# Optimization experiments

Measured on AMD Instinct MI355X. Metric: run time of the kernel, lower is better.

The kernel has to match this reference:

```python
import jax, jax.numpy as jnp
import numpy as np

N, E, DIM, H, EDIM = 50000, 800000, 128, 4, 16
C = DIM // H  # per-head channels = 32

def _ln(x, g, b, eps=1e-5):
    mu = jnp.mean(x, -1, keepdims=True)
    var = jnp.mean((x - mu) ** 2, -1, keepdims=True)
    return (x - mu) * jax.lax.rsqrt(var + eps) * g + b

def setup_inputs() -> dict:
    key = jax.random.key(0)
    ks = jax.random.split(key, 16)
    s = lambda d: 1.0 / np.sqrt(d)
    inp = {
        'x': jax.random.normal(ks[0], (N, DIM), jnp.float32),
        'edge_index_s': jax.random.randint(ks[1], (2, E), 0, N, jnp.int64),
        'edge_attr_s': jax.random.normal(ks[2], (E, EDIM), jnp.float32),
        'Wq': jax.random.normal(ks[3], (DIM, DIM), jnp.float32) * s(DIM),
        'bq': jnp.zeros((DIM,), jnp.float32),
        'Wk': jax.random.normal(ks[4], (DIM, DIM), jnp.float32) * s(DIM),
        'bk': jnp.zeros((DIM,), jnp.float32),
        'Wv': jax.random.normal(ks[5], (DIM, DIM), jnp.float32) * s(DIM),
        'bv': jnp.zeros((DIM,), jnp.float32),
        'We': jax.random.normal(ks[6], (EDIM, DIM), jnp.float32) * s(EDIM),
        'be': jnp.zeros((DIM,), jnp.float32),
        'Ws': jax.random.normal(ks[7], (DIM, DIM), jnp.float32) * s(DIM),
        'bs': jnp.zeros((DIM,), jnp.float32),
        'Wbeta': jax.random.normal(ks[8], (3 * DIM, 1), jnp.float32) * s(3 * DIM),
        'g1': jnp.ones((DIM,), jnp.float32),
        'b1': jnp.zeros((DIM,), jnp.float32),
        'Wf1': jax.random.normal(ks[9], (DIM, 4 * DIM), jnp.float32) * s(DIM),
        'bf1': jnp.zeros((4 * DIM,), jnp.float32),
        'Wf2': jax.random.normal(ks[10], (4 * DIM, DIM), jnp.float32) * s(4 * DIM),
        'bf2': jnp.zeros((DIM,), jnp.float32),
        'g2': jnp.ones((DIM,), jnp.float32),
        'b2': jnp.zeros((DIM,), jnp.float32),
    }
    return inp

def reference(x, edge_index_s, edge_attr_s, Wq, bq, Wk, bk, Wv, bv, We, be,
              Ws, bs, Wbeta, g1, b1, Wf1, bf1, Wf2, bf2, g2, b2):
    src, dst = edge_index_s[0], edge_index_s[1]
    # project + reshape to [N, H, C]
    q = (x @ Wq + bq).reshape(N, H, C)
    k = (x @ Wk + bk).reshape(N, H, C)
    v = (x @ Wv + bv).reshape(N, H, C)
    e = (edge_attr_s @ We + be).reshape(E, H, C)
    # gather along edges (irregular access)
    kj = k[src] + e  # [E, H, C]
    vj = v[src] + e
    alpha = jnp.einsum('ehc,ehc->eh', q[dst], kj) / jnp.sqrt(jnp.float32(C))
    # segment softmax over incoming edges of each dst node
    m = jax.ops.segment_max(alpha, dst, num_segments=N)  # [N, H]
    a = jnp.exp(alpha - m[dst])
    denom = jax.ops.segment_sum(a, dst, num_segments=N)
    a = a / (denom[dst] + 1e-16)
    out = jax.ops.segment_sum(a[:, :, None] * vj, dst, num_segments=N)  # [N, H, C]
    out = out.reshape(N, DIM)
    # beta-gated skip (TransformerConv beta=True)
    xr = x @ Ws + bs
    beta = jax.nn.sigmoid(jnp.concatenate([out, xr, out - xr], -1) @ Wbeta)  # [N, 1]
    xs = beta * xr + (1.0 - beta) * out
    # residual + LN + FFN + LN
    h = _ln(x + xs, g1, b1)
    ff = jax.nn.relu(h @ Wf1 + bf1) @ Wf2 + bf2
    return _ln(h + ff, g2, b2)
```

## Files before the change

### kernel.cpp

```cpp
#include <hip/hip_runtime.h>
#include <hip/hip_bf16.h>

#define NN 50000
#define EE 800000
#define DIMM 128

typedef __attribute__((ext_vector_type(8))) short bf16x8;
typedef __attribute__((ext_vector_type(8))) unsigned short us8;
typedef __attribute__((ext_vector_type(4))) float f32x4;

static __device__ __forceinline__ unsigned short f2bf(float f) {
    unsigned int u = __float_as_uint(f);
    unsigned int r = (u + 0x7fffu + ((u >> 16) & 1u)) >> 16;
    return (unsigned short)r;
}
static __device__ __forceinline__ float bf2f(unsigned short s) {
    return __uint_as_float(((unsigned int)s) << 16);
}

#define RED16(v) do { int _t; \
    _t = __builtin_amdgcn_update_dpp(0, __float_as_int(v), 0x128, 0xF, 0xF, true); v += __int_as_float(_t); \
    _t = __builtin_amdgcn_update_dpp(0, __float_as_int(v), 0x124, 0xF, 0xF, true); v += __int_as_float(_t); \
    _t = __builtin_amdgcn_update_dpp(0, __float_as_int(v), 0x122, 0xF, 0xF, true); v += __int_as_float(_t); \
    _t = __builtin_amdgcn_update_dpp(0, __float_as_int(v), 0x121, 0xF, 0xF, true); v += __int_as_float(_t); \
} while (0)

__global__ __launch_bounds__(256) void pack_w(
    const float* __restrict__ Wq, const float* __restrict__ Wk,
    const float* __restrict__ Wv, const float* __restrict__ Ws,
    const float* __restrict__ bq, const float* __restrict__ bk,
    const float* __restrict__ bv, const float* __restrict__ bs,
    const float* __restrict__ Wf1, const float* __restrict__ Wf2,
    unsigned short* __restrict__ wqkvsT, unsigned short* __restrict__ wf1T,
    unsigned short* __restrict__ wf2T, float* __restrict__ biasq)
{
    int i = blockIdx.x * 256 + threadIdx.x;
    if (i < 65536) {
        int n = i >> 7, k = i & 127;
        int sel = n >> 7, col = n & 127;
        const float* W = sel == 0 ? Wq : sel == 1 ? Wk : sel == 2 ? Wv : Ws;
        wqkvsT[i] = f2bf(W[k * 128 + col]);
    } else if (i < 131072) {
        int j = i - 65536; int n = j >> 7, k = j & 127;
        wf1T[j] = f2bf(Wf1[k * 512 + n]);
    } else if (i < 196608) {
        int j = i - 131072; int n = j >> 9, k = j & 511;
        wf2T[j] = f2bf(Wf2[k * 128 + n]);
    } else if (i < 197120) {
        int j = i - 196608; int sel = j >> 7;
        const float* bp = sel == 0 ? bq : sel == 1 ? bk : sel == 2 ? bv : bs;
        biasq[j] = bp[j & 127];
    }
}

template<bool A_BF16, int EPI>
__global__ __launch_bounds__(256) void gemm_k(
    const void* __restrict__ Ap, const unsigned short* __restrict__ Bt,
    const float* __restrict__ bias, void* __restrict__ Cp,
    float* __restrict__ qb, unsigned short* __restrict__ kvb, float* __restrict__ xrb,
    int M, int Nn, int K)
{
    __shared__ unsigned short As[128][72];
    __shared__ unsigned short Bs[128][72];
    int tid = threadIdx.x;
    int nb = Nn >> 7;
    int bm = blockIdx.x / nb, bn = blockIdx.x % nb;
    int w = tid >> 6, lane = tid & 63;
    int wm = w >> 1, wn = w & 1;
    int lr = lane & 15, quad = lane >> 4;

    f32x4 acc[4][4];
    #pragma unroll
    for (int i = 0; i < 4; i++)
        #pragma unroll
        for (int j = 0; j < 4; j++) { f32x4 z = {0.f, 0.f, 0.f, 0.f}; acc[i][j] = z; }

    for (int kc = 0; kc < K; kc += 64) {
        #pragma unroll
        for (int it = 0; it < 4; ++it) {
            int row = it * 32 + (tid >> 3);
            int k8 = (tid & 7) * 8;
            int rg = bm * 128 + row;
            us8 st = {0, 0, 0, 0, 0, 0, 0, 0};
            if (rg < M) {
                if constexpr (A_BF16) {
                    st = *(const us8*)((const unsigned short*)Ap + (size_t)rg * K + kc + k8);
                } else {
                    const float* src = (const float*)Ap + (size_t)rg * K + kc + k8;
                    float4 f0 = *(const float4*)src;
                    float4 f1 = *(const float4*)(src + 4);
                    st[0] = f2bf(f0.x); st[1] = f2bf(f0.y); st[2] = f2bf(f0.z); st[3] = f2bf(f0.w);
                    st[4] = f2bf(f1.x); st[5] = f2bf(f1.y); st[6] = f2bf(f1.z); st[7] = f2bf(f1.w);
                }
            }
            *(us8*)&As[row][k8] = st;
            *(us8*)&Bs[row][k8] = *(const us8*)(Bt + (size_t)(bn * 128 + row) * K + kc + k8);
        }
        __syncthreads();
        #pragma unroll
        for (int kk = 0; kk < 2; ++kk) {
            bf16x8 af[4], bfr[4];
            #pragma unroll
            for (int mi = 0; mi < 4; mi++)
                af[mi] = *(const bf16x8*)&As[wm * 64 + mi * 16 + lr][kk * 32 + quad * 8];
            #pragma unroll
            for (int ni = 0; ni < 4; ni++)
                bfr[ni] = *(const bf16x8*)&Bs[wn * 64 + ni * 16 + lr][kk * 32 + quad * 8];
            #pragma unroll
            for (int mi = 0; mi < 4; mi++)
                #pragma unroll
                for (int ni = 0; ni < 4; ni++)
                    acc[mi][ni] = __builtin_amdgcn_mfma_f32_16x16x32_bf16(af[mi], bfr[ni], acc[mi][ni], 0, 0, 0);
        }
        __syncthreads();
    }
    #pragma unroll
    for (int mi = 0; mi < 4; mi++) {
        #pragma unroll
        for (int ni = 0; ni < 4; ni++) {
            int cg = bn * 128 + wn * 64 + ni * 16 + lr;
            float bv = bias[cg];
            #pragma unroll
            for (int r = 0; r < 4; r++) {
                int rg = bm * 128 + wm * 64 + mi * 16 + quad * 4 + r;
                if (rg < M) {
                    float val = acc[mi][ni][r] + bv;
                    if constexpr (EPI == 0) {
                        ((float*)Cp)[(size_t)rg * Nn + cg] = val;
                    } else if constexpr (EPI == 1) {
                        val = fmaxf(val, 0.f);
                        ((unsigned short*)Cp)[(size_t)rg * Nn + cg] = f2bf(val);
                    } else {
                        int sel = cg >> 7, c = cg & 127;
                        if (sel == 0)      qb[(size_t)rg * 128 + c] = val;
                        else if (sel == 1) kvb[(size_t)rg * 256 + 2 * c] = f2bf(val);
                        else if (sel == 2) kvb[(size_t)rg * 256 + 2 * c + 1] = f2bf(val);
                        else               xrb[(size_t)rg * 128 + c] = val;
                    }
                }
            }
        }
    }
}

__global__ __launch_bounds__(256) void qwe_k(
    const float* __restrict__ q, const float* __restrict__ We,
    float* __restrict__ qweb)
{
    int wave = threadIdx.x >> 6, lane = threadIdx.x & 63;
    int n = blockIdx.x * 4 + wave;
    if (n >= NN) return;
    int head = lane >> 4, j = lane & 15;
    const float* qp = q + (size_t)n * 128 + head * 32;
    const float* wp = We + j * 128 + head * 32;
    float acc = 0.f;
    #pragma unroll
    for (int c = 0; c < 32; c += 4) {
        float4 qv = *(const float4*)(qp + c);
        float4 wv = *(const float4*)(wp + c);
        acc += qv.x * wv.x + qv.y * wv.y + qv.z * wv.z + qv.w * wv.w;
    }
    qweb[(size_t)n * 64 + lane] = acc * 0.17677669529663687f;
}

__global__ __launch_bounds__(256) void hist_k(const int* __restrict__ dst, int* __restrict__ deg) {
    int e = blockIdx.x * 256 + threadIdx.x;
    if (e < EE) atomicAdd(&deg[dst[e]], 1);
}

__global__ __launch_bounds__(256) void scan_phaseA(const int* __restrict__ deg, int* __restrict__ rs,
                                                   int* __restrict__ bsum) {
    __shared__ int sm[256];
    int tid = threadIdx.x;
    int i = blockIdx.x * 256 + tid;
    int v = (i < NN) ? deg[i] : 0;
    sm[tid] = v;
    __syncthreads();
    #pragma unroll
    for (int off = 1; off < 256; off <<= 1) {
        int t = 0;
        if (tid >= off) t = sm[tid - off];
        __syncthreads();
        if (tid >= off) sm[tid] += t;
        __syncthreads();
    }
    if (i < NN) rs[i] = sm[tid] - v;
    if (tid == 255) bsum[blockIdx.x] = sm[255];
}

__global__ __launch_bounds__(256) void scan_phaseB(int* __restrict__ bsum, int nb) {
    __shared__ int sm[256];
    int tid = threadIdx.x;
    int v = (tid < nb) ? bsum[tid] : 0;
    sm[tid] = v;
    __syncthreads();
    #pragma unroll
    for (int off = 1; off < 256; off <<= 1) {
        int t = 0;
        if (tid >= off) t = sm[tid - off];
        __syncthreads();
        if (tid >= off) sm[tid] += t;
        __syncthreads();
    }
    if (tid < nb) bsum[tid] = sm[tid] - v;
}

__global__ __launch_bounds__(256) void scan_phaseC(int* __restrict__ rs, const int* __restrict__ bsum) {
    int i = blockIdx.x * 256 + threadIdx.x;
    if (i < NN) rs[i] += bsum[blockIdx.x];
    if (i == 0) rs[NN] = EE;
}

__global__ __launch_bounds__(256) void scatter_k(
    const int* __restrict__ src, const int* __restrict__ dst,
    const float* __restrict__ eattr, const int* __restrict__ rs,
    int* __restrict__ cur, int* __restrict__ srcs_sorted,
    unsigned short* __restrict__ eas)
{
    int e = blockIdx.x * 256 + threadIdx.x;
    if (e < EE) {
        int d = dst[e];
        int p = atomicAdd(&cur[d], 1);
        int pos = rs[d] + p;
        srcs_sorted[pos] = src[e];
        const float* ap = eattr + (size_t)e * 16;
        float4 a0 = *(const float4*)ap;
        float4 a1 = *(const float4*)(ap + 4);
        float4 a2 = *(const float4*)(ap + 8);
        float4 a3 = *(const float4*)(ap + 12);
        us8 lo, hi;
        lo[0] = f2bf(a0.x); lo[1] = f2bf(a0.y); lo[2] = f2bf(a0.z); lo[3] = f2bf(a0.w);
        lo[4] = f2bf(a1.x); lo[5] = f2bf(a1.y); lo[6] = f2bf(a1.z); lo[7] = f2bf(a1.w);
        hi[0] = f2bf(a2.x); hi[1] = f2bf(a2.y); hi[2] = f2bf(a2.z); hi[3] = f2bf(a2.w);
        hi[4] = f2bf(a3.x); hi[5] = f2bf(a3.y); hi[6] = f2bf(a3.z); hi[7] = f2bf(a3.w);
        *(us8*)(eas + (size_t)pos * 16)     = lo;
        *(us8*)(eas + (size_t)pos * 16 + 8) = hi;
    }
}

__global__ __launch_bounds__(256, 4) void attn_kernel(
    const float* __restrict__ q, const unsigned int* __restrict__ kvb,
    const float* __restrict__ xr, const float* __restrict__ x,
    const unsigned short* __restrict__ eas, const int* __restrict__ srcs,
    const int* __restrict__ rs, const float* __restrict__ qweb,
    const float* __restrict__ We, const float* __restrict__ be,
    const float* __restrict__ Wbeta,
    const float* __restrict__ gamma1, const float* __restrict__ beta1,
    float* __restrict__ hout, unsigned int* __restrict__ hbf)
{
    int wave = threadIdx.x >> 6;
    int lane = threadIdx.x & 63;
    int n = blockIdx.x * 4 + wave;
    if (n >= NN) return;
    int c0 = lane * 2, c1 = c0 + 1;
    int jlane = lane & 15;
    int hbase = lane & 48;

    float be0 = be[c0], be1 = be[c1];

    float2 q2 = *(const float2*)(q + (size_t)n * 128 + c0);
    q2.x *= 0.17677669529663687f;
    q2.y *= 0.17677669529663687f;

    float qbe = q2.x * be0 + q2.y * be1;
    RED16(qbe);
    float qwe = qweb[(size_t)n * 64 + lane];

    float l = 0.f, a0 = 0.f, a1 = 0.f, s = 0.f;
    int beg = rs[n], end = rs[n + 1];

    int sr0[8], sr1[8];
    unsigned short ea0[8], ea1[8];
    uint2 kv0[8], kv1[8];

#define LOADMETA(g, SR, EA) { \
    _Pragma("unroll") \
    for (int j = 0; j < 8; j++) { \
        int idx = min((g) + j, EE - 1); \
        SR[j] = srcs[idx]; \
        EA[j] = eas[(size_t)idx * 16 + jlane]; \
    } }
#define GATHER(SR, KV) { \
    _Pragma("unroll") \
    for (int j = 0; j < 8; j++) \
        KV[j] = *(const uint2*)(kvb + (size_t)SR[j] * 128 + (lane << 1)); }
#define COMPUTE(g, EA, KV) { \
    int cnt = end - (g); \
    _Pragma("unroll") \
    for (int j = 0; j < 8; j++) { \
        if (j < cnt) { \
            float ea = bf2f(EA[j]); \
            unsigned int kx = KV[j].x, ky = KV[j].y; \
            float k0 = __uint_as_float(kx << 16); \
            float v0 = __uint_as_float(kx & 0xffff0000u); \
            float k1 = __uint_as_float(ky << 16); \
            float v1 = __uint_as_float(ky & 0xffff0000u); \
            float part = fmaf(q2.x, k0, fmaf(q2.y, k1, qwe * ea)); \
            RED16(part); \
            float wgt = __expf(part + qbe); \
            l += wgt; \
            a0 = fmaf(wgt, v0, a0); \
            a1 = fmaf(wgt, v1, a1); \
            s = fmaf(wgt, ea, s); \
        } } }

    if (beg < end) {
        LOADMETA(beg, sr0, ea0)
        GATHER(sr0, kv0)
        for (int g = beg; ; g += 16) {
            bool m1 = (g + 8 < end);
            if (m1) { LOADMETA(g + 8, sr1, ea1) GATHER(sr1, kv1) }
            COMPUTE(g, ea0, kv0)
            if (!m1) break;
            bool m2 = (g + 16 < end);
            if (m2) { LOADMETA(g + 16, sr0, ea0) GATHER(sr0, kv0) }
            COMPUTE(g + 8, ea1, kv1)
            if (!m2) break;
        }
    }
#undef LOADMETA
#undef GATHER
#undef COMPUTE

    float eo0 = l * be0, eo1 = l * be1;
    #pragma unroll
    for (int j = 0; j < 16; j++) {
        float sj = __shfl(s, hbase + j);
        eo0 = fmaf(sj, We[j * 128 + c0], eo0);
        eo1 = fmaf(sj, We[j * 128 + c1], eo1);
    }
    a0 += eo0; a1 += eo1;

    float inv = l > 0.f ? 1.f / l : 0.f;
    float o0 = a0 * inv, o1 = a1 * inv;

    float wbo0 = Wbeta[c0],        wbo1 = Wbeta[c1];
    float wbx0 = Wbeta[128 + c0],  wbx1 = Wbeta[128 + c1];
    float wbd0 = Wbeta[256 + c0],  wbd1 = Wbeta[256 + c1];
    float2 xr2 = *(const float2*)(xr + (size_t)n * 128 + c0);
    float bl = o0 * wbo0 + o1 * wbo1 + xr2.x * wbx0 + xr2.y * wbx1
             + (o0 - xr2.x) * wbd0 + (o1 - xr2.y) * wbd1;
    #pragma unroll
    for (int off = 1; off < 64; off <<= 1) bl += __shfl_xor(bl, off);
    float beta = 1.f / (1.f + __expf(-bl));
    float xs0 = beta * xr2.x + (1.f - beta) * o0;
    float xs1 = beta * xr2.y + (1.f - beta) * o1;

    float2 xv = *(const float2*)(x + (size_t)n * 128 + c0);
    float t0 = xv.x + xs0, t1 = xv.y + xs1;
    float sm = t0 + t1;
    #pragma unroll
    for (int off = 1; off < 64; off <<= 1) sm += __shfl_xor(sm, off);
    float mu = sm * (1.f / 128.f);
    float d0 = t0 - mu, d1 = t1 - mu;
    float vv = d0 * d0 + d1 * d1;
    #pragma unroll
    for (int off = 1; off < 64; off <<= 1) vv += __shfl_xor(vv, off);
    float is = rsqrtf(vv * (1.f / 128.f) + 1e-5f);
    float h0 = d0 * is * gamma1[c0] + beta1[c0];
    float h1 = d1 * is * gamma1[c1] + beta1[c1];
    *(float2*)(hout + (size_t)n * 128 + c0) = make_float2(h0, h1);
    hbf[(size_t)n * 64 + lane] = (unsigned int)f2bf(h0) | ((unsigned int)f2bf(h1) << 16);
}

__global__ __launch_bounds__(256) void ln2_k(
    const float* __restrict__ h, const float* __restrict__ ff2,
    const float* __restrict__ gamma2, const float* __restrict__ beta2,
    float* __restrict__ out)
{
    int wave = threadIdx.x >> 6;
    int lane = threadIdx.x & 63;
    int n = blockIdx.x * 4 + wave;
    if (n >= NN) return;
    int c0 = lane * 2;
    float2 hv = *(const float2*)(h + (size_t)n * 128 + c0);
    float2 fv = *(const float2*)(ff2 + (size_t)n * 128 + c0);
    float t0 = hv.x + fv.x, t1 = hv.y + fv.y;
    float sm = t0 + t1;
    #pragma unroll
    for (int off = 1; off < 64; off <<= 1) sm += __shfl_xor(sm, off);
    float mu = sm * (1.f / 128.f);
    float d0 = t0 - mu, d1 = t1 - mu;
    float vv = d0 * d0 + d1 * d1;
    #pragma unroll
    for (int off = 1; off < 64; off <<= 1) vv += __shfl_xor(vv, off);
    float is = rsqrtf(vv * (1.f / 128.f) + 1e-5f);
    float o0 = d0 * is * gamma2[c0] + beta2[c0];
    float o1 = d1 * is * gamma2[c0 + 1] + beta2[c0 + 1];
    *(float2*)(out + (size_t)n * 128 + c0) = make_float2(o0, o1);
}

extern "C" void kernel_launch(void* const* d_in, const int* in_sizes, int n_in,
                              void* d_out, int out_size, void* d_ws, size_t ws_size,
                              hipStream_t stream) {
    const float* x      = (const float*)d_in[0];
    const int*   eindex = (const int*)d_in[1];
    const float* eattr  = (const float*)d_in[2];
    const float* Wq = (const float*)d_in[3];  const float* bq = (const float*)d_in[4];
    const float* Wk = (const float*)d_in[5];  const float* bk = (const float*)d_in[6];
    const float* Wv = (const float*)d_in[7];  const float* bv = (const float*)d_in[8];
    const float* We = (const float*)d_in[9];  const float* be = (const float*)d_in[10];
    const float* Ws = (const float*)d_in[11]; const float* bs = (const float*)d_in[12];
    const float* Wbeta = (const float*)d_in[13];
    const float* g1 = (const float*)d_in[14]; const float* b1 = (const float*)d_in[15];
    const float* Wf1 = (const float*)d_in[16]; const float* bf1 = (const float*)d_in[17];
    const float* Wf2 = (const float*)d_in[18]; const float* bf2 = (const float*)d_in[19];
    const float* g2 = (const float*)d_in[20]; const float* b2 = (const float*)d_in[21];

    char* ws = (char*)d_ws;
    size_t off = 0;
    #define ALLOC(ptr, type, bytes) type* ptr = (type*)(ws + off); off = (off + (size_t)(bytes) + 255) & ~(size_t)255;
    ALLOC(wqkvsT, unsigned short, 512 * 128 * 2)
    ALLOC(wf1T,   unsigned short, 512 * 128 * 2)
    ALLOC(wf2T,   unsigned short, 128 * 512 * 2)
    ALLOC(biasq,  float,          512 * 4)
    ALLOC(qb,     float,          (size_t)NN * 128 * 4)
    ALLOC(kvb,    unsigned short, (size_t)NN * 256 * 2)
    ALLOC(xrb,    float,          (size_t)NN * 128 * 4)
    ALLOC(h,      float,          (size_t)NN * 128 * 4)
    ALLOC(hbf,    unsigned int,   (size_t)NN * 128 * 2)
    ALLOC(qweb,   float,          (size_t)NN * 64 * 4)
    ALLOC(deg,    int,            2 * NN * 4)
    ALLOC(row_start, int,         (NN + 1) * 4)
    ALLOC(bsum,   int,            1024)
    ALLOC(srcs_sorted, int,       (size_t)EE * 4)
    ALLOC(eas,    unsigned short, (size_t)EE * 16 * 2)
    #undef ALLOC
    int* cursor = deg + NN;
    unsigned short* ff1 = (unsigned short*)qb;
    float* ff2 = xrb;

    hipMemsetAsync(deg, 0, (size_t)2 * NN * 4, stream);

    pack_w<<<770, 256, 0, stream>>>(Wq, Wk, Wv, Ws, bq, bk, bv, bs, Wf1, Wf2,
                                    wqkvsT, wf1T, wf2T, biasq);

    gemm_k<false, 2><<<391 * 4, 256, 0, stream>>>(x, wqkvsT, biasq, nullptr,
                                                  qb, kvb, xrb, NN, 512, 128);

    qwe_k<<<12500, 256, 0, stream>>>(qb, We, qweb);

    hist_k<<<3125, 256, 0, stream>>>(eindex + EE, deg);
    scan_phaseA<<<196, 256, 0, stream>>>(deg, row_start, bsum);
    scan_phaseB<<<1, 256, 0, stream>>>(bsum, 196);
    scan_phaseC<<<196, 256, 0, stream>>>(row_start, bsum);
    scatter_k<<<3125, 256, 0, stream>>>(eindex, eindex + EE, eattr, row_start,
                                        cursor, srcs_sorted, eas);

    attn_kernel<<<12500, 256, 0, stream>>>(qb, (const unsigned int*)kvb, xrb, x,
                                           eas, srcs_sorted, row_start, qweb,
                                           We, be, Wbeta, g1, b1, h, hbf);

    gemm_k<true, 1><<<391 * 4, 256, 0, stream>>>(hbf, wf1T, bf1, ff1,
                                                 nullptr, nullptr, nullptr, NN, 512, 128);
    gemm_k<true, 0><<<391 * 1, 256, 0, stream>>>(ff1, wf2T, bf2, ff2,
                                                 nullptr, nullptr, nullptr, NN, 128, 512);

    ln2_k<<<12500, 256, 0, stream>>>(h, ff2, g2, b2, (float*)d_out);
}
```

Baseline: 523.9 us.

## Fold q·We projection into QKV GEMM and fuse LayerNorm2 into FFN2 epilogue

Precomputes Wq·We and Wq·be, scaled by 1/sqrt(C), as 68 extra output columns of the packed QKV weight. The first GEMM then emits qwe and qbe directly, which removes the separate qwe_k kernel and the per-node qbe reduction in attention. The second FFN GEMM now adds the residual h and the bias and computes LayerNorm in its epilogue, using DPP reductions plus shared memory across the two column-waves. This removes the ln2_k kernel and the ff2 round trip through memory, at the cost of a wider first GEMM (640 columns, 60 of them padding), bf16 rounding of the folded weights, and a one-pass variance formula.

```diff
diff --git a/kernel.cpp b/kernel.cpp
--- a/kernel.cpp
+++ b/kernel.cpp
@@ -25,31 +25,67 @@
     _t = __builtin_amdgcn_update_dpp(0, __float_as_int(v), 0x121, 0xF, 0xF, true); v += __int_as_float(_t); \
 } while (0)
 
+#define QSCALE 0.17677669529663687f
+
 __global__ __launch_bounds__(256) void pack_w(
     const float* __restrict__ Wq, const float* __restrict__ Wk,
     const float* __restrict__ Wv, const float* __restrict__ Ws,
     const float* __restrict__ bq, const float* __restrict__ bk,
     const float* __restrict__ bv, const float* __restrict__ bs,
     const float* __restrict__ Wf1, const float* __restrict__ Wf2,
+    const float* __restrict__ We, const float* __restrict__ be,
     unsigned short* __restrict__ wqkvsT, unsigned short* __restrict__ wf1T,
     unsigned short* __restrict__ wf2T, float* __restrict__ biasq)
 {
     int i = blockIdx.x * 256 + threadIdx.x;
-    if (i < 65536) {
+    if (i < 81920) {
         int n = i >> 7, k = i & 127;
-        int sel = n >> 7, col = n & 127;
-        const float* W = sel == 0 ? Wq : sel == 1 ? Wk : sel == 2 ? Wv : Ws;
-        wqkvsT[i] = f2bf(W[k * 128 + col]);
-    } else if (i < 131072) {
-        int j = i - 65536; int n = j >> 7, k = j & 127;
+        unsigned short outv = 0;
+        if (n < 512) {
+            int sel = n >> 7, col = n & 127;
+            const float* W = sel == 0 ? Wq : sel == 1 ? Wk : sel == 2 ? Wv : Ws;
+            outv = f2bf(W[k * 128 + col]);
+        } else if (n < 576) {
+            int m = n - 512, head = m >> 4, j = m & 15;
+            float acc = 0.f;
+            for (int c = 0; c < 32; c++)
+                acc += Wq[k * 128 + head * 32 + c] * We[j * 128 + head * 32 + c];
+            outv = f2bf(acc * QSCALE);
+        } else if (n < 580) {
+            int head = n - 576;
+            float acc = 0.f;
+            for (int c = 0; c < 32; c++)
+                acc += Wq[k * 128 + head * 32 + c] * be[head * 32 + c];
+            outv = f2bf(acc * QSCALE);
+        }
+        wqkvsT[i] = outv;
+    } else if (i < 147456) {
+        int j = i - 81920; int n = j >> 7, k = j & 127;
         wf1T[j] = f2bf(Wf1[k * 512 + n]);
-    } else if (i < 196608) {
-        int j = i - 131072; int n = j >> 9, k = j & 511;
+    } else if (i < 212992) {
+        int j = i - 147456; int n = j >> 9, k = j & 511;
         wf2T[j] = f2bf(Wf2[k * 128 + n]);
-    } else if (i < 197120) {
-        int j = i - 196608; int sel = j >> 7;
-        const float* bp = sel == 0 ? bq : sel == 1 ? bk : sel == 2 ? bv : bs;
-        biasq[j] = bp[j & 127];
+    } else if (i < 213632) {
+        int j = i - 212992;
+        float bvv = 0.f;
+        if (j < 512) {
+            int sel = j >> 7;
+            const float* bp = sel == 0 ? bq : sel == 1 ? bk : sel == 2 ? bv : bs;
+            bvv = bp[j & 127];
+        } else if (j < 576) {
+            int m = j - 512, head = m >> 4, jj = m & 15;
+            float acc = 0.f;
+            for (int c = 0; c < 32; c++)
+                acc += bq[head * 32 + c] * We[jj * 128 + head * 32 + c];
+            bvv = acc * QSCALE;
+        } else if (j < 580) {
+            int head = j - 576;
+            float acc = 0.f;
+            for (int c = 0; c < 32; c++)
+                acc += bq[head * 32 + c] * be[head * 32 + c];
+            bvv = acc * QSCALE;
+        }
+        biasq[j] = bvv;
     }
 }
 
@@ -58,10 +94,14 @@
     const void* __restrict__ Ap, const unsigned short* __restrict__ Bt,
     const float* __restrict__ bias, void* __restrict__ Cp,
     float* __restrict__ qb, unsigned short* __restrict__ kvb, float* __restrict__ xrb,
+    float* __restrict__ qweb, float* __restrict__ qbeb,
+    const float* __restrict__ hb, const float* __restrict__ g2, const float* __restrict__ b2,
     int M, int Nn, int K)
 {
     __shared__ unsigned short As[128][72];
     __shared__ unsigned short Bs[128][72];
+    __shared__ float lsum[2][128];
+    __shared__ float lsq[2][128];
     int tid = threadIdx.x;
     int nb = Nn >> 7;
     int bm = blockIdx.x / nb, bn = blockIdx.x % nb;
@@ -114,6 +154,72 @@
         }
         __syncthreads();
     }
+
+    if constexpr (EPI == 3) {
+        #pragma unroll
+        for (int mi = 0; mi < 4; mi++) {
+            #pragma unroll
+            for (int ni = 0; ni < 4; ni++) {
+                int cg = wn * 64 + ni * 16 + lr;
+                float bv = bias[cg];
+                #pragma unroll
+                for (int r = 0; r < 4; r++) {
+                    int rg = bm * 128 + wm * 64 + mi * 16 + quad * 4 + r;
+                    float hv = (rg < M) ? hb[(size_t)rg * 128 + cg] : 0.f;
+                    acc[mi][ni][r] += bv + hv;
+                }
+            }
+        }
+        float prs[4][4], prq[4][4];
+        #pragma unroll
+        for (int mi = 0; mi < 4; mi++)
+            #pragma unroll
+            for (int r = 0; r < 4; r++) {
+                float sm = 0.f, sq = 0.f;
+                #pragma unroll
+                for (int ni = 0; ni < 4; ni++) {
+                    float t = acc[mi][ni][r];
+                    sm += t; sq += t * t;
+                }
+                RED16(sm); RED16(sq);
+                prs[mi][r] = sm; prq[mi][r] = sq;
+            }
+        if (lr == 0) {
+            #pragma unroll
+            for (int mi = 0; mi < 4; mi++)
+                #pragma unroll
+                for (int r = 0; r < 4; r++) {
+                    int row = wm * 64 + mi * 16 + quad * 4 + r;
+                    lsum[wn][row] = prs[mi][r];
+                    lsq[wn][row]  = prq[mi][r];
+                }
+        }
+        __syncthreads();
+        float* outp = (float*)Cp;
+        #pragma unroll
+        for (int mi = 0; mi < 4; mi++) {
+            #pragma unroll
+            for (int ni = 0; ni < 4; ni++) {
+                int cg = wn * 64 + ni * 16 + lr;
+                float gv = g2[cg], bv2 = b2[cg];
+                #pragma unroll
+                for (int r = 0; r < 4; r++) {
+                    int row = wm * 64 + mi * 16 + quad * 4 + r;
+                    int rg = bm * 128 + row;
+                    if (rg < M) {
+                        float tot = lsum[0][row] + lsum[1][row];
+                        float tq  = lsq[0][row] + lsq[1][row];
+                        float mu = tot * (1.f / 128.f);
+                        float var = tq * (1.f / 128.f) - mu * mu;
+                        float is = rsqrtf(var + 1e-5f);
+                        outp[(size_t)rg * 128 + cg] = (acc[mi][ni][r] - mu) * is * gv + bv2;
+                    }
+                }
+            }
+        }
+        return;
+    }
+
     #pragma unroll
     for (int mi = 0; mi < 4; mi++) {
         #pragma unroll
@@ -135,32 +241,16 @@
                         if (sel == 0)      qb[(size_t)rg * 128 + c] = val;
                         else if (sel == 1) kvb[(size_t)rg * 256 + 2 * c] = f2bf(val);
                         else if (sel == 2) kvb[(size_t)rg * 256 + 2 * c + 1] = f2bf(val);
-                        else               xrb[(size_t)rg * 128 + c] = val;
+                        else if (sel == 3) xrb[(size_t)rg * 128 + c] = val;
+                        else {
+                            if (c < 64)      qweb[(size_t)rg * 64 + c] = val;
+                            else if (c < 68) qbeb[(size_t)rg * 4 + (c - 64)] = val;
+                        }
                     }
                 }
             }
         }
     }
-}
-
-__global__ __launch_bounds__(256) void qwe_k(
-    const float* __restrict__ q, const float* __restrict__ We,
-    float* __restrict__ qweb)
-{
-    int wave = threadIdx.x >> 6, lane = threadIdx.x & 63;
-    int n = blockIdx.x * 4 + wave;
-    if (n >= NN) return;
-    int head = lane >> 4, j = lane & 15;
-    const float* qp = q + (size_t)n * 128 + head * 32;
-    const float* wp = We + j * 128 + head * 32;
-    float acc = 0.f;
-    #pragma unroll
-    for (int c = 0; c < 32; c += 4) {
-        float4 qv = *(const float4*)(qp + c);
-        float4 wv = *(const float4*)(wp + c);
-        acc += qv.x * wv.x + qv.y * wv.y + qv.z * wv.z + qv.w * wv.w;
-    }
-    qweb[(size_t)n * 64 + lane] = acc * 0.17677669529663687f;
 }
 
 __global__ __launch_bounds__(256) void hist_k(const int* __restrict__ dst, int* __restrict__ deg) {
@@ -243,6 +333,7 @@
     const float* __restrict__ xr, const float* __restrict__ x,
     const unsigned short* __restrict__ eas, const int* __restrict__ srcs,
     const int* __restrict__ rs, const float* __restrict__ qweb,
+    const float* __restrict__ qbeb,
     const float* __restrict__ We, const float* __restrict__ be,
     const float* __restrict__ Wbeta,
     const float* __restrict__ gamma1, const float* __restrict__ beta1,
@@ -256,15 +347,12 @@
     int jlane = lane & 15;
     int hbase = lane & 48;
 
-    float be0 = be[c0], be1 = be[c1];
-
     float2 q2 = *(const float2*)(q + (size_t)n * 128 + c0);
-    q2.x *= 0.17677669529663687f;
-    q2.y *= 0.17677669529663687f;
-
-    float qbe = q2.x * be0 + q2.y * be1;
-    RED16(qbe);
+    q2.x *= QSCALE;
+    q2.y *= QSCALE;
+
     float qwe = qweb[(size_t)n * 64 + lane];
+    float qbe = qbeb[(size_t)n * 4 + (lane >> 4)];
 
     float l = 0.f, a0 = 0.f, a1 = 0.f, s = 0.f;
     int beg = rs[n], end = rs[n + 1];
@@ -322,6 +410,7 @@
 #undef GATHER
 #undef COMPUTE
 
+    float be0 = be[c0], be1 = be[c1];
     float eo0 = l * be0, eo1 = l * be1;
     #pragma unroll
     for (int j = 0; j < 16; j++) {
@@ -361,33 +450,6 @@
     float h1 = d1 * is * gamma1[c1] + beta1[c1];
     *(float2*)(hout + (size_t)n * 128 + c0) = make_float2(h0, h1);
     hbf[(size_t)n * 64 + lane] = (unsigned int)f2bf(h0) | ((unsigned int)f2bf(h1) << 16);
-}
-
-__global__ __launch_bounds__(256) void ln2_k(
-    const float* __restrict__ h, const float* __restrict__ ff2,
-    const float* __restrict__ gamma2, const float* __restrict__ beta2,
-    float* __restrict__ out)
-{
-    int wave = threadIdx.x >> 6;
-    int lane = threadIdx.x & 63;
-    int n = blockIdx.x * 4 + wave;
-    if (n >= NN) return;
-    int c0 = lane * 2;
-    float2 hv = *(const float2*)(h + (size_t)n * 128 + c0);
-    float2 fv = *(const float2*)(ff2 + (size_t)n * 128 + c0);
-    float t0 = hv.x + fv.x, t1 = hv.y + fv.y;
-    float sm = t0 + t1;
-    #pragma unroll
-    for (int off = 1; off < 64; off <<= 1) sm += __shfl_xor(sm, off);
-    float mu = sm * (1.f / 128.f);
-    float d0 = t0 - mu, d1 = t1 - mu;
-    float vv = d0 * d0 + d1 * d1;
-    #pragma unroll
-    for (int off = 1; off < 64; off <<= 1) vv += __shfl_xor(vv, off);
-    float is = rsqrtf(vv * (1.f / 128.f) + 1e-5f);
-    float o0 = d0 * is * gamma2[c0] + beta2[c0];
-    float o1 = d1 * is * gamma2[c0 + 1] + beta2[c0 + 1];
-    *(float2*)(out + (size_t)n * 128 + c0) = make_float2(o0, o1);
 }
 
 extern "C" void kernel_launch(void* const* d_in, const int* in_sizes, int n_in,
@@ -410,16 +472,17 @@
     char* ws = (char*)d_ws;
     size_t off = 0;
     #define ALLOC(ptr, type, bytes) type* ptr = (type*)(ws + off); off = (off + (size_t)(bytes) + 255) & ~(size_t)255;
-    ALLOC(wqkvsT, unsigned short, 512 * 128 * 2)
+    ALLOC(wqkvsT, unsigned short, 640 * 128 * 2)
     ALLOC(wf1T,   unsigned short, 512 * 128 * 2)
     ALLOC(wf2T,   unsigned short, 128 * 512 * 2)
-    ALLOC(biasq,  float,          512 * 4)
+    ALLOC(biasq,  float,          640 * 4)
     ALLOC(qb,     float,          (size_t)NN * 128 * 4)
     ALLOC(kvb,    unsigned short, (size_t)NN * 256 * 2)
     ALLOC(xrb,    float,          (size_t)NN * 128 * 4)
     ALLOC(h,      float,          (size_t)NN * 128 * 4)
     ALLOC(hbf,    unsigned int,   (size_t)NN * 128 * 2)
     ALLOC(qweb,   float,          (size_t)NN * 64 * 4)
+    ALLOC(qbeb,   float,          (size_t)NN * 4 * 4)
     ALLOC(deg,    int,            2 * NN * 4)
     ALLOC(row_start, int,         (NN + 1) * 4)
     ALLOC(bsum,   int,            1024)
@@ -428,17 +491,15 @@
     #undef ALLOC
     int* cursor = deg + NN;
     unsigned short* ff1 = (unsigned short*)qb;
-    float* ff2 = xrb;
 
     hipMemsetAsync(deg, 0, (size_t)2 * NN * 4, stream);
 
-    pack_w<<<770, 256, 0, stream>>>(Wq, Wk, Wv, Ws, bq, bk, bv, bs, Wf1, Wf2,
+    pack_w<<<835, 256, 0, stream>>>(Wq, Wk, Wv, Ws, bq, bk, bv, bs, Wf1, Wf2, We, be,
                                     wqkvsT, wf1T, wf2T, biasq);
 
-    gemm_k<false, 2><<<391 * 4, 256, 0, stream>>>(x, wqkvsT, biasq, nullptr,
-                                                  qb, kvb, xrb, NN, 512, 128);
-
-    qwe_k<<<12500, 256, 0, stream>>>(qb, We, qweb);
+    gemm_k<false, 2><<<391 * 5, 256, 0, stream>>>(x, wqkvsT, biasq, nullptr,
+                                                  qb, kvb, xrb, qweb, qbeb,
+                                                  nullptr, nullptr, nullptr, NN, 640, 128);
 
     hist_k<<<3125, 256, 0, stream>>>(eindex + EE, deg);
     scan_phaseA<<<196, 256, 0, stream>>>(deg, row_start, bsum);
@@ -448,13 +509,13 @@
                                         cursor, srcs_sorted, eas);
 
     attn_kernel<<<12500, 256, 0, stream>>>(qb, (const unsigned int*)kvb, xrb, x,
-                                           eas, srcs_sorted, row_start, qweb,
+                                           eas, srcs_sorted, row_start, qweb, qbeb,
                                            We, be, Wbeta, g1, b1, h, hbf);
 
     gemm_k<true, 1><<<391 * 4, 256, 0, stream>>>(hbf, wf1T, bf1, ff1,
+                                                 nullptr, nullptr, nullptr, nullptr, nullptr,
                                                  nullptr, nullptr, nullptr, NN, 512, 128);
-    gemm_k<true, 0><<<391 * 1, 256, 0, stream>>>(ff1, wf2T, bf2, ff2,
-                                                 nullptr, nullptr, nullptr, NN, 128, 512);
-
-    ln2_k<<<12500, 256, 0, stream>>>(h, ff2, g2, b2, (float*)d_out);
-}
+    gemm_k<true, 3><<<391, 256, 0, stream>>>(ff1, wf2T, bf2, d_out,
+                                             nullptr, nullptr, nullptr, nullptr, nullptr,
+                                             h, g2, b2, NN, 128, 512);
+}
```

Measured after the change: 497.8 us. 1.05x faster.
